# Optimization experiments

Measured on AMD Instinct MI355X. Metric: run time of the kernel, lower is better.

Reference implementation:

```python
import jax, jax.numpy as jnp
import numpy as np
from jax import lax

H = 32          # hidden per direction (HIDDENDIM // 2)
T = 8192        # tokens
M = 12          # morphemes per token
INP = 100       # word2vec dim (LSTMINPDIM)
DP_V, DPD = 40, 4
TAGS = 44


def _lstm_dir(x, h0, c0, Wih, Whh, b, reverse):
    """Single-direction LSTM over x: [S, D]. PyTorch gate order i,f,g,o."""
    def step(carry, xt):
        h, c = carry
        g = xt @ Wih.T + h @ Whh.T + b
        i, f, gg, o = jnp.split(g, 4, axis=-1)
        c = jax.nn.sigmoid(f) * c + jax.nn.sigmoid(i) * jnp.tanh(gg)
        h = jax.nn.sigmoid(o) * jnp.tanh(c)
        return (h, c), h
    xs = jnp.flip(x, 0) if reverse else x
    (hN, cN), hs = lax.scan(step, (h0, c0), xs)
    if reverse:
        hs = jnp.flip(hs, 0)
    return hs, hN, cN


def _bilstm(x, h0, c0, layers):
    """2-layer bidirectional LSTM. h0/c0: [4, H], PyTorch order (layer*2+dir).
    layers: list of (Wih[2,4H,Din], Whh[2,4H,H], b[2,4H]) per layer (b = b_ih+b_hh)."""
    out = x
    hs, cs = [], []
    for l, (Wih, Whh, b) in enumerate(layers):
        f_hs, f_h, f_c = _lstm_dir(out, h0[2 * l], c0[2 * l], Wih[0], Whh[0], b[0], False)
        b_hs, b_h, b_c = _lstm_dir(out, h0[2 * l + 1], c0[2 * l + 1], Wih[1], Whh[1], b[1], True)
        out = jnp.concatenate([f_hs, b_hs], axis=-1)
        hs += [f_h, b_h]
        cs += [f_c, b_c]
    return out, jnp.stack(hs), jnp.stack(cs)


def setup_inputs() -> dict:
    key = jax.random.key(0)
    ks = jax.random.split(key, 20)
    k = 1.0 / np.sqrt(H)
    u = lambda kk, shp: jax.random.uniform(kk, shp, jnp.float32, -k, k)
    inp = {
        "morp_embs": jax.random.normal(ks[0], (T, M, INP), jnp.float32),
        "feat_vectors": jax.random.uniform(ks[1], (T, 1), jnp.float32),
        "dp_emb": jax.random.normal(ks[2], (DP_V, DPD), jnp.float32),
        "m_Wih0": u(ks[3], (2, 4 * H, INP)),
        "m_Whh0": u(ks[4], (2, 4 * H, H)),
        "m_b0": u(ks[5], (2, 4 * H)),
        "m_Wih1": u(ks[6], (2, 4 * H, 2 * H)),
        "m_Whh1": u(ks[7], (2, 4 * H, H)),
        "m_b1": u(ks[8], (2, 4 * H)),
        "t_Wih0": u(ks[9], (2, 4 * H, 2 * H + DPD + 1)),
        "t_Whh0": u(ks[10], (2, 4 * H, H)),
        "t_b0": u(ks[11], (2, 4 * H)),
        "t_Wih1": u(ks[12], (2, 4 * H, 2 * H)),
        "t_Whh1": u(ks[13], (2, 4 * H, H)),
        "t_b1": u(ks[14], (2, 4 * H)),
        "W_out": u(ks[15], (TAGS, 2 * H)),
        "b_out": u(ks[16], (TAGS,)),
        "dp_in": jax.random.randint(ks[17], (T,), 0, DP_V, jnp.int32),
        "mask": jax.random.randint(ks[18], (T,), 0, 2, jnp.int32),
    }
    return inp


def reference(morp_embs, feat_vectors, dp_emb,
              m_Wih0, m_Whh0, m_b0, m_Wih1, m_Whh1, m_b1,
              t_Wih0, t_Whh0, t_b0, t_Wih1, t_Whh1, t_b1,
              W_out, b_out, dp_in, mask):
    dtype = morp_embs.dtype
    morp_layers = [(m_Wih0, m_Whh0, m_b0), (m_Wih1, m_Whh1, m_b1)]
    tok_layers = [(t_Wih0, t_Whh0, t_b0), (t_Wih1, t_Whh1, t_b1)]
    z = jnp.zeros((4, H), dtype)

    # morpheme-level LSTM: hidden state is carried across tokens, as in the
    # original (self.hidden_lstm_morp is threaded through the python loop)
    def tok_step(carry, xm):
        h, c = carry
        out, hN, cN = _bilstm(xm, h, c, morp_layers)   # out: [M, 2H]
        return (hN, cN), out[-1]                        # last morpheme output

    _, tok_vec = lax.scan(tok_step, (z, z), morp_embs)  # [T, 2H]

    input_embs = jnp.concatenate([tok_vec, dp_emb[dp_in], feat_vectors], axis=1)  # [T, 69]
    tok_out, _, _ = _bilstm(input_embs, z, z, tok_layers)  # [T, 2H]

    tag_space = tok_out @ W_out.T + b_out  # [T, TAGS]
    # where mask <= 0, force last logit to 1 (pre-relu), as in the python loop
    tag_space = tag_space.at[:, -1].set(
        jnp.where(mask > 0, tag_space[:, -1], jnp.asarray(1.0, dtype)))
    tag_space = jax.nn.relu(tag_space)
    return jax.nn.softmax(tag_space, axis=1)
```

## Files before the change

### kernel.cpp

```cpp
#include <hip/hip_runtime.h>

#define T_TOK   8192
#define M_MORPH 12
#define NMORPH  (T_TOK * M_MORPH)

typedef float f32x4 __attribute__((ext_vector_type(4)));
typedef float f32x2 __attribute__((ext_vector_type(2)));
typedef short s16x8 __attribute__((ext_vector_type(8)));

__device__ __forceinline__ float sigmoidf_(float x) {
    return __fdividef(1.f, 1.f + __expf(-x));
}

__device__ __forceinline__ int rowof(int s, int mode, int N) {
    if (mode == 0) return s;
    if (mode == 1) { int m = s % M_MORPH; return s + (M_MORPH - 1) - 2 * m; }
    return N - 1 - s;
}

#define PKFMA(acc, w, h) \
    asm("v_pk_fma_f32 %0, %1, %2, %0" : "+v"(acc) : "v"(w), "v"(h))

__device__ __forceinline__ void half_swap(float v, float& lo_b, float& hi_b) {
#if __has_builtin(__builtin_amdgcn_permlane32_swap)
    auto r = __builtin_amdgcn_permlane32_swap(__float_as_uint(v), __float_as_uint(v),
                                              false, false);
    lo_b = __uint_as_float((unsigned)r[0]);
    hi_b = __uint_as_float((unsigned)r[1]);
#else
    const float e = __shfl_xor(v, 32);
    const bool lo = ((threadIdx.x & 63) < 32);
    lo_b = lo ? v : e;
    hi_b = lo ? e : v;
#endif
}

__global__ void prep_B(const float* __restrict__ W, const float* __restrict__ b,
                       unsigned short* __restrict__ Bh, unsigned short* __restrict__ Bl,
                       float* __restrict__ bcat, int WK, int KPAD) {
    const int n = blockIdx.x;
    const int k = threadIdx.x;
    const int dir = n >> 7, r = n & 127;
    float v = (k < WK) ? W[(size_t)(dir * 128 + r) * WK + k] : 0.f;
    unsigned int u = __float_as_uint(v);
    unsigned short hb = (unsigned short)(u >> 16);
    float fh = __uint_as_float(u & 0xFFFF0000u);
    float lo = v - fh;
    unsigned short lb = (unsigned short)(__float_as_uint(lo) >> 16);
    Bh[(size_t)n * KPAD + k] = hb;
    Bl[(size_t)n * KPAD + k] = lb;
    if (k == 0) bcat[n] = b[dir * 128 + r];
}

template <int KACT, int KPAD, int AS>
__global__ __launch_bounds__(256, 2) void gemm_mfma(const float* __restrict__ A,
                                                    const unsigned short* __restrict__ Bh,
                                                    const unsigned short* __restrict__ Bl,
                                                    const float* __restrict__ bc,
                                                    float* __restrict__ X) {
    const int lane = threadIdx.x & 63;
    const int wave = threadIdx.x >> 6;
    const int col = lane & 15;
    const int kc  = (lane >> 4) * 8;
    const int row0 = blockIdx.x * 128 + wave * 32;

    f32x4 acc[2][16];
#pragma unroll
    for (int ct = 0; ct < 16; ++ct) {
        const float bv = bc[ct * 16 + col];
        f32x4 v; v[0] = bv; v[1] = bv; v[2] = bv; v[3] = bv;
        acc[0][ct] = v; acc[1][ct] = v;
    }

    const float* a0 = A + (size_t)(row0 + col) * AS;
    const float* a1 = A + (size_t)(row0 + 16 + col) * AS;

#pragma unroll
    for (int ks = 0; ks < KPAD / 32; ++ks) {
        const int kb = ks * 32 + kc;
        s16x8 ah[2], al[2];
#pragma unroll
        for (int rt = 0; rt < 2; ++rt) {
            const float* ap = (rt ? a1 : a0) + kb;
            float av[8];
#pragma unroll
            for (int h = 0; h < 2; ++h) {
                float4 t; t.x = t.y = t.z = t.w = 0.f;
                if ((ks + 1) * 32 <= KACT || kb + h * 4 < KACT)
                    t = *(const float4*)(ap + h * 4);
                av[h * 4 + 0] = t.x; av[h * 4 + 1] = t.y;
                av[h * 4 + 2] = t.z; av[h * 4 + 3] = t.w;
            }
#pragma unroll
            for (int j = 0; j < 8; ++j) {
                const unsigned int u = __float_as_uint(av[j]);
                const unsigned short hb = (unsigned short)(u >> 16);
                const float fh = __uint_as_float(u & 0xFFFF0000u);
                const float lov = av[j] - fh;
                const unsigned short lb = (unsigned short)(__float_as_uint(lov) >> 16);
                ah[rt][j] = (short)hb;
                al[rt][j] = (short)lb;
            }
        }

        const unsigned short* bhp = Bh + (size_t)col * KPAD + kb;
        const unsigned short* blp = Bl + (size_t)col * KPAD + kb;
#pragma unroll
        for (int ct = 0; ct < 16; ++ct) {
            const s16x8 bh8 = *(const s16x8*)(bhp + (size_t)ct * 16 * KPAD);
            const s16x8 bl8 = *(const s16x8*)(blp + (size_t)ct * 16 * KPAD);
#pragma unroll
            for (int rt = 0; rt < 2; ++rt) {
                acc[rt][ct] = __builtin_amdgcn_mfma_f32_16x16x32_bf16(ah[rt], bh8, acc[rt][ct], 0, 0, 0);
                acc[rt][ct] = __builtin_amdgcn_mfma_f32_16x16x32_bf16(ah[rt], bl8, acc[rt][ct], 0, 0, 0);
                acc[rt][ct] = __builtin_amdgcn_mfma_f32_16x16x32_bf16(al[rt], bh8, acc[rt][ct], 0, 0, 0);
            }
        }
    }

    const int r_in = (lane >> 4) * 4;
#pragma unroll
    for (int rt = 0; rt < 2; ++rt)
#pragma unroll
        for (int g = 0; g < 2; ++g)
#pragma unroll
            for (int ct2 = 0; ct2 < 4; ++ct2) {
                const int ct = g * 8 + ct2;
                const int c  = ct * 16 + col;
                const int cm = c & 127;
                const int nc = g * 128 + cm * 2;
#pragma unroll
                for (int i = 0; i < 4; ++i) {
                    f32x2 v2;
                    v2[0] = acc[rt][ct][i];
                    v2[1] = acc[rt][ct + 4][i];
                    *(f32x2*)&X[(size_t)(row0 + rt * 16 + r_in + i) * 256 + nc] = v2;
                }
            }
}

template <int DM, int SL>
__device__ __forceinline__ void chain_body(
    const float* __restrict__ Xc, float* __restrict__ HoutLane,
    const bool lo, const int lane,
    f32x2 (&wa)[16], f32x2 (&wb)[16], float* sh,
    const int N, const int cs, const int ce, const int ws)
{
    const float cg = lo ? 2.f : 1.f;
    const float ca = lo ? -1.f : 0.f;

    f32x2 q[8];
#pragma unroll
    for (int p = 0; p < 8; ++p) {
        const int rp = rowof(ws + p, DM, N);
        q[p] = *(const f32x2*)(Xc + (size_t)rp * 256);
    }

    int mp = (ws + 8) % M_MORPH;
    int pb;
    {
        const int sp0 = ws + 8;
        int rp0;
        if (DM == 1)      rp0 = sp0 + 11 - 2 * mp;
        else if (DM == 2) rp0 = N - 1 - sp0;
        else              rp0 = sp0;
        pb = rp0 * 1024;
    }

    int ms = ws % M_MORPH;
    int rs;
    if (DM == 1)      rs = ws + 11 - 2 * ms;
    else if (DM == 2) rs = N - 1 - ws;
    else              rs = ws;
    int tk = ws / M_MORPH;

    float hreg = 0.f, c = 0.f;

#pragma unroll 1
    for (int s = ws; s < ce; s += 8) {
#pragma unroll
        for (int u = 0; u < 8; ++u) {
            const int su = s + u;
            const float x1 = q[u][0], x2 = q[u][1];

            {
                const int sp = su + 8;
                const int ob = (sp < ce) ? pb : 0;
                q[u] = *(const f32x2*)((const char*)Xc + ob);
                if (DM == 1) {
                    if (mp == 11) { mp = 0; pb += 23 * 1024; }
                    else          { ++mp; pb -= 1024; }
                } else if (DM == 2) { pb -= 1024; }
                else                { pb += 1024; }
            }

            sh[lane] = hreg;
            f32x4 hq[8];
            {
                const f32x4* s4 = (const f32x4*)sh;
#pragma unroll
                for (int i = 0; i < 8; ++i) hq[i] = s4[i];
            }

            f32x2 a01 = {x1, 0.f}, a23 = {0.f, 0.f};
            f32x2 b01 = {x2, 0.f}, b23 = {0.f, 0.f};
#pragma unroll
            for (int i = 0; i < 8; ++i) {
                f32x2 hlo = __builtin_shufflevector(hq[i], hq[i], 0, 1);
                f32x2 hhi = __builtin_shufflevector(hq[i], hq[i], 2, 3);
                PKFMA(a01, wa[2 * i],     hlo);
                PKFMA(a23, wa[2 * i + 1], hhi);
                PKFMA(b01, wb[2 * i],     hlo);
                PKFMA(b23, wb[2 * i + 1], hhi);
            }
            const float g1 = (a01[0] + a01[1]) + (a23[0] + a23[1]);
            const float g2 = (b01[0] + b01[1]) + (b23[0] + b23[1]);

            const float s1 = sigmoidf_(g1);
            const float uu = sigmoidf_(cg * g2);
            const float t2 = fmaf(cg, uu, ca);

            float si, sf, tg, so;
            half_swap(s1, si, sf);
            half_swap(t2, tg, so);

            c = sf * c + si * tg;
            const float th = 2.f * sigmoidf_(2.f * c) - 1.f;
            hreg = so * th;

            if (!SL) {
                if (su >= cs) {
                    if (lo) HoutLane[(size_t)rs * 64] = hreg;
                }
            } else {
                const bool last = (DM == 1) ? (ms == 0) : (ms == 11);
                if (su >= cs && last) {
                    if (lo) HoutLane[(size_t)tk * 64] = hreg;
                }
            }

            if (DM == 1) {
                if (ms == 11) { ms = 0; ++tk; rs += 23; }
                else          { ++ms; --rs; }
            } else if (DM == 2) {
                --rs;
            } else {
                ++rs;
                if (SL) { if (ms == 11) { ms = 0; ++tk; } else ++ms; }
            }
        }
    }
}

template <int BDM, int SL>
__global__ __launch_bounds__(64)
__attribute__((amdgpu_waves_per_eu(2, 2)))
void lstm_chain_t(const float* __restrict__ Xall,
                  const float* __restrict__ Whhall,
                  float* __restrict__ Hout,
                  int N, int Lc, int Wu) {
    __shared__ __align__(16) float sh[64];
    const int lane = threadIdx.x;
    const int dir = blockIdx.y;
    const float* Whh = Whhall + dir * 128 * 32;

    const int cs = blockIdx.x * Lc;
    if (cs >= N) return;
    int ce = cs + Lc; if (ce > N) ce = N;
    int ws = cs - Wu; if (ws < 0) ws = 0;

    f32x2 wa[16], wb[16];
    {
        const f32x2* w1 = (const f32x2*)(Whh + lane * 32);
        const f32x2* w2 = (const f32x2*)(Whh + (lane + 64) * 32);
#pragma unroll
        for (int i = 0; i < 16; ++i) { wa[i] = w1[i]; wb[i] = w2[i]; }
    }
#pragma unroll
    for (int i = 0; i < 16; ++i) {
        asm volatile("" : "+v"(wa[i]));
        asm volatile("" : "+v"(wb[i]));
    }

    const float* Xc = Xall + dir * 128 + lane * 2;
    float* HoutLane = Hout + dir * 32 + lane;
    const bool lo = (lane < 32);

    if (dir == 0)
        chain_body<0,   SL>(Xc, HoutLane, lo, lane, wa, wb, sh, N, cs, ce, ws);
    else
        chain_body<BDM, SL>(Xc, HoutLane, lo, lane, wa, wb, sh, N, cs, ce, ws);
}

__global__ __launch_bounds__(256) void build_embs(const float* __restrict__ tokvec,
                                                  const float* __restrict__ dp_emb,
                                                  const int* __restrict__ dp_in,
                                                  const float* __restrict__ feat,
                                                  float* __restrict__ embs) {
    const int idx = blockIdx.x * 256 + threadIdx.x;
    if (idx >= T_TOK * 96) return;
    const int t = idx / 96, i = idx % 96;
    float v;
    if (i < 64)      v = tokvec[(size_t)t * 64 + i];
    else if (i < 68) v = dp_emb[dp_in[t] * 4 + (i - 64)];
    else if (i == 68) v = feat[t];
    else             v = 0.f;
    embs[idx] = v;
}

__global__ __launch_bounds__(256) void epilogue_k(const float* __restrict__ Ht1,
                                                  const float* __restrict__ Wout,
                                                  const float* __restrict__ bout,
                                                  const int* __restrict__ maskp,
                                                  float* __restrict__ out) {
    const int wid = threadIdx.x >> 6;
    const int lane = threadIdx.x & 63;
    const int t = blockIdx.x * 4 + wid;
    float acc = -1e30f;
    if (lane < 44) {
        acc = bout[lane];
        const float* wr = Wout + lane * 64;
        const float* hr = Ht1 + (size_t)t * 64;
#pragma unroll
        for (int k = 0; k < 64; ++k) acc += hr[k] * wr[k];
        if (lane == 43 && maskp[t] <= 0) acc = 1.0f;
        acc = fmaxf(acc, 0.f);
    }
    float mx = acc;
#pragma unroll
    for (int off = 32; off >= 1; off >>= 1) mx = fmaxf(mx, __shfl_xor(mx, off));
    const float e = (lane < 44) ? __expf(acc - mx) : 0.f;
    float ssum = e;
#pragma unroll
    for (int off = 32; off >= 1; off >>= 1) ssum += __shfl_xor(ssum, off);
    if (lane < 44) out[(size_t)t * 44 + lane] = e / ssum;
}

extern "C" void kernel_launch(void* const* d_in, const int* in_sizes, int n_in,
                              void* d_out, int out_size, void* d_ws, size_t ws_size,
                              hipStream_t stream) {
    const float* morp  = (const float*)d_in[0];
    const float* feat  = (const float*)d_in[1];
    const float* dpemb = (const float*)d_in[2];
    const float* mWih0 = (const float*)d_in[3];
    const float* mWhh0 = (const float*)d_in[4];
    const float* mb0   = (const float*)d_in[5];
    const float* mWih1 = (const float*)d_in[6];
    const float* mWhh1 = (const float*)d_in[7];
    const float* mb1   = (const float*)d_in[8];
    const float* tWih0 = (const float*)d_in[9];
    const float* tWhh0 = (const float*)d_in[10];
    const float* tb0   = (const float*)d_in[11];
    const float* tWih1 = (const float*)d_in[12];
    const float* tWhh1 = (const float*)d_in[13];
    const float* tb1   = (const float*)d_in[14];
    const float* Wout  = (const float*)d_in[15];
    const float* bout  = (const float*)d_in[16];
    const int*   dpin  = (const int*)d_in[17];
    const int*   maskp = (const int*)d_in[18];
    float* out = (float*)d_out;

    float* w = (float*)d_ws;
    size_t off = 0;
    float* X0     = w + off; off += (size_t)NMORPH * 256;
    float* Hcat0  = w + off; off += (size_t)NMORPH * 64;
    float* tokvec = w + off; off += (size_t)T_TOK * 64;
    float* embs   = w + off; off += (size_t)T_TOK * 96;
    float* Ht0    = w + off; off += (size_t)T_TOK * 64;
    float* Ht1    = w + off; off += (size_t)T_TOK * 64;
    unsigned short* Bh = (unsigned short*)(w + off); off += 256 * 128 / 2;
    unsigned short* Bl = (unsigned short*)(w + off); off += 256 * 128 / 2;
    float* bcat   = w + off; off += 256;
    float* Xt = X0;
    (void)ws_size; (void)in_sizes; (void)n_in; (void)out_size;

    prep_B<<<256, 128, 0, stream>>>(mWih0, mb0, Bh, Bl, bcat, 100, 128);
    gemm_mfma<100, 128, 100><<<NMORPH / 128, 256, 0, stream>>>(morp, Bh, Bl, bcat, X0);
    lstm_chain_t<1, 0><<<dim3(NMORPH / 96, 2), 64, 0, stream>>>(X0, mWhh0, Hcat0, NMORPH, 96, 64);
    prep_B<<<256, 64, 0, stream>>>(mWih1, mb1, Bh, Bl, bcat, 64, 64);
    gemm_mfma<64, 64, 64><<<NMORPH / 128, 256, 0, stream>>>(Hcat0, Bh, Bl, bcat, X0);
    lstm_chain_t<1, 1><<<dim3(NMORPH / 96, 2), 64, 0, stream>>>(X0, mWhh1, tokvec, NMORPH, 96, 64);

    build_embs<<<(T_TOK * 96) / 256, 256, 0, stream>>>(tokvec, dpemb, dpin, feat, embs);
    prep_B<<<256, 96, 0, stream>>>(tWih0, tb0, Bh, Bl, bcat, 69, 96);
    gemm_mfma<96, 96, 96><<<T_TOK / 128, 256, 0, stream>>>(embs, Bh, Bl, bcat, Xt);
    lstm_chain_t<2, 0><<<dim3(T_TOK / 32, 2), 64, 0, stream>>>(Xt, tWhh0, Ht0, T_TOK, 32, 64);
    prep_B<<<256, 64, 0, stream>>>(tWih1, tb1, Bh, Bl, bcat, 64, 64);
    gemm_mfma<64, 64, 64><<<T_TOK / 128, 256, 0, stream>>>(Ht0, Bh, Bl, bcat, Xt);
    lstm_chain_t<2, 0><<<dim3(T_TOK / 32, 2), 64, 0, stream>>>(Xt, tWhh1, Ht1, T_TOK, 32, 64);

    epilogue_k<<<T_TOK / 4, 256, 0, stream>>>(Ht1, Wout, bout, maskp, out);
}
```

Before: 405.9 us.

## Batch morpheme LSTM recurrences into MFMA across 16 chunks per wave

Replaces the per-lane scalar packed-FMA recurrence for the two morpheme-level LSTM layers with a new kernel in which each wave runs 16 independent sequence chunks as the columns of bf16 split-precision MFMAs (hi/lo split of Whh and h). The hidden state is redistributed through a small LDS tile each step, the gate inputs are prefetched two steps ahead, and inactive steps during warmup are written to a dump buffer. The GEMM gains a template flag so the morpheme path stores X in natural column order, matching the new kernel's layout. This aims to cut the serial FMA work and launch far fewer waves. In exchange it adds LDS round-trips and bf16 split conversion on every step, plus three MFMAs per gate tile.

```diff
diff --git a/kernel.cpp b/kernel.cpp
--- a/kernel.cpp
+++ b/kernel.cpp
@@ -33,6 +33,17 @@
     lo_b = lo ? v : e;
     hi_b = lo ? e : v;
 #endif
+}
+
+__device__ __forceinline__ void bf16_split_pair(float x0, float x1,
+                                                unsigned& hi, unsigned& lo) {
+    const unsigned u0 = __float_as_uint(x0);
+    const unsigned u1 = __float_as_uint(x1);
+    hi = (u0 >> 16) | (u1 & 0xFFFF0000u);
+    const float h0 = __uint_as_float(u0 & 0xFFFF0000u);
+    const float h1 = __uint_as_float(u1 & 0xFFFF0000u);
+    lo = (__float_as_uint(x0 - h0) >> 16)
+       | (__float_as_uint(x1 - h1) & 0xFFFF0000u);
 }
 
 __global__ void prep_B(const float* __restrict__ W, const float* __restrict__ b,
@@ -52,7 +63,7 @@
     if (k == 0) bcat[n] = b[dir * 128 + r];
 }
 
-template <int KACT, int KPAD, int AS>
+template <int KACT, int KPAD, int AS, bool PAIRED>
 __global__ __launch_bounds__(256, 2) void gemm_mfma(const float* __restrict__ A,
                                                     const unsigned short* __restrict__ Bh,
                                                     const unsigned short* __restrict__ Bl,
@@ -119,24 +130,212 @@
     }
 
     const int r_in = (lane >> 4) * 4;
-#pragma unroll
-    for (int rt = 0; rt < 2; ++rt)
-#pragma unroll
-        for (int g = 0; g < 2; ++g)
-#pragma unroll
-            for (int ct2 = 0; ct2 < 4; ++ct2) {
-                const int ct = g * 8 + ct2;
-                const int c  = ct * 16 + col;
-                const int cm = c & 127;
-                const int nc = g * 128 + cm * 2;
-#pragma unroll
-                for (int i = 0; i < 4; ++i) {
-                    f32x2 v2;
-                    v2[0] = acc[rt][ct][i];
-                    v2[1] = acc[rt][ct + 4][i];
-                    *(f32x2*)&X[(size_t)(row0 + rt * 16 + r_in + i) * 256 + nc] = v2;
+    if constexpr (!PAIRED) {
+#pragma unroll
+        for (int rt = 0; rt < 2; ++rt)
+#pragma unroll
+            for (int ct = 0; ct < 16; ++ct)
+#pragma unroll
+                for (int i = 0; i < 4; ++i)
+                    X[(size_t)(row0 + rt * 16 + r_in + i) * 256 + ct * 16 + col] = acc[rt][ct][i];
+    } else {
+#pragma unroll
+        for (int rt = 0; rt < 2; ++rt)
+#pragma unroll
+            for (int g = 0; g < 2; ++g)
+#pragma unroll
+                for (int ct2 = 0; ct2 < 4; ++ct2) {
+                    const int ct = g * 8 + ct2;
+                    const int c  = ct * 16 + col;
+                    const int cm = c & 127;
+                    const int nc = g * 128 + cm * 2;
+#pragma unroll
+                    for (int i = 0; i < 4; ++i) {
+                        f32x2 v2;
+                        v2[0] = acc[rt][ct][i];
+                        v2[1] = acc[rt][ct + 4][i];
+                        *(f32x2*)&X[(size_t)(row0 + rt * 16 + r_in + i) * 256 + nc] = v2;
+                    }
                 }
-            }
+    }
+}
+
+template <int DM, int SL>
+__device__ __forceinline__ void mstep(
+    const char* __restrict__ xb, char* __restrict__ hb,
+    float* __restrict__ dl, float* __restrict__ Hls,
+    const int col, const int rg,
+    const s16x8 (&wh)[8], const s16x8 (&wl)[8],
+    s16x8& bh, s16x8& bl,
+    f32x4 (&q)[8], f32x4 (&cst)[2],
+    int& su, const int cs, const int ce,
+    int& pf_b, int& m_pf,
+    int& st_b, int& m_st, int& tk_b)
+{
+    f32x4 acc[8];
+#pragma unroll
+    for (int tt = 0; tt < 8; ++tt) {
+        acc[tt] = __builtin_amdgcn_mfma_f32_16x16x32_bf16(wh[tt], bh, q[tt], 0, 0, 0);
+        acc[tt] = __builtin_amdgcn_mfma_f32_16x16x32_bf16(wh[tt], bl, acc[tt], 0, 0, 0);
+        acc[tt] = __builtin_amdgcn_mfma_f32_16x16x32_bf16(wl[tt], bh, acc[tt], 0, 0, 0);
+    }
+
+    {
+        const char* xp = xb + pf_b;
+#pragma unroll
+        for (int tt = 0; tt < 8; ++tt)
+            q[tt] = *(const f32x4*)(xp + tt * 64);
+        if (DM == 1) {
+            const bool w = (m_pf == 11);
+            pf_b += w ? 23 * 1024 : -1024;
+            m_pf = w ? 0 : m_pf + 1;
+        } else {
+            pf_b += 1024;
+        }
+    }
+
+    f32x4 v0, v1;
+#pragma unroll
+    for (int p = 0; p < 2; ++p) {
+#pragma unroll
+        for (int r = 0; r < 4; ++r) {
+            const float gi = acc[0 + p][r], gf = acc[2 + p][r];
+            const float gg = acc[4 + p][r], go = acc[6 + p][r];
+            const float si = sigmoidf_(gi);
+            const float sf = sigmoidf_(gf);
+            const float tg = 2.f * sigmoidf_(2.f * gg) - 1.f;
+            const float so = sigmoidf_(go);
+            const float cn = sf * cst[p][r] + si * tg;
+            cst[p][r] = cn;
+            const float th = 2.f * sigmoidf_(2.f * cn) - 1.f;
+            const float hv = so * th;
+            if (p == 0) v0[r] = hv; else v1[r] = hv;
+        }
+    }
+
+    {
+        bool act = (su >= cs) && (su < ce);
+        if (SL) act = act && ((DM == 1) ? (m_st == 0) : (m_st == 11));
+        char* base = hb + (SL ? tk_b : st_b);
+        float* a0 = act ? (float*)base : dl;
+        float* a1 = act ? (float*)(base + 64) : (dl + 4);
+        *(f32x4*)a0 = v0;
+        *(f32x4*)a1 = v1;
+
+        ++su;
+        if (DM == 1) {
+            const bool w = (m_st == 11);
+            st_b += w ? 23 * 256 : -256;
+            if (SL) tk_b += w ? 256 : 0;
+            m_st = w ? 0 : m_st + 1;
+        } else {
+            st_b += 256;
+            if (SL) {
+                const bool w = (m_st == 11);
+                tk_b += w ? 256 : 0;
+                m_st = w ? 0 : m_st + 1;
+            }
+        }
+    }
+
+    *(f32x4*)&Hls[col * 36 + 4 * rg]      = v0;
+    *(f32x4*)&Hls[col * 36 + 16 + 4 * rg] = v1;
+    const f32x4 r0 = *(const f32x4*)&Hls[col * 36 + 8 * rg];
+    const f32x4 r1 = *(const f32x4*)&Hls[col * 36 + 8 * rg + 4];
+    union { s16x8 s; unsigned u[4]; } BH, BL;
+    bf16_split_pair(r0[0], r0[1], BH.u[0], BL.u[0]);
+    bf16_split_pair(r0[2], r0[3], BH.u[1], BL.u[1]);
+    bf16_split_pair(r1[0], r1[1], BH.u[2], BL.u[2]);
+    bf16_split_pair(r1[2], r1[3], BH.u[3], BL.u[3]);
+    bh = BH.s; bl = BL.s;
+}
+
+template <int DM, int SL>
+__device__ __forceinline__ void mrun(
+    const float* __restrict__ Xn, const float* __restrict__ Wd,
+    float* __restrict__ Hout, float* __restrict__ dump,
+    float* __restrict__ Hls,
+    const int dir, const int col, const int rg, const int lane,
+    const int N, const int Lc, const int Wu, const int nsteps)
+{
+    const int g  = blockIdx.x * 16 + col;
+    const int cs = g * Lc;
+    const int ce = cs + Lc;
+    const int off = (g == 0) ? 0 : cs - Wu;
+
+    s16x8 wh[8], wl[8];
+#pragma unroll
+    for (int tt = 0; tt < 8; ++tt) {
+        const float* wr = Wd + (size_t)(tt * 16 + col) * 32 + rg * 8;
+        const float4 w0 = *(const float4*)(wr);
+        const float4 w1 = *(const float4*)(wr + 4);
+        union { s16x8 s; unsigned u[4]; } H_, L_;
+        bf16_split_pair(w0.x, w0.y, H_.u[0], L_.u[0]);
+        bf16_split_pair(w0.z, w0.w, H_.u[1], L_.u[1]);
+        bf16_split_pair(w1.x, w1.y, H_.u[2], L_.u[2]);
+        bf16_split_pair(w1.z, w1.w, H_.u[3], L_.u[3]);
+        wh[tt] = H_.s; wl[tt] = L_.s;
+    }
+
+    const char* xb = (const char*)Xn + dir * 512 + rg * 16;
+    char* hb = (char*)Hout + (size_t)(dir * 32 + 4 * rg) * 4;
+    float* dl = dump + ((size_t)(blockIdx.x * 2 + dir) * 64 + lane) * 8;
+
+    int m = off % 12;
+    int rb = ((DM == 1) ? (off + 11 - 2 * m) : off) * 1024;
+    f32x4 q0[8], q1[8];
+    {
+        const char* xp = xb + rb;
+#pragma unroll
+        for (int tt = 0; tt < 8; ++tt) q0[tt] = *(const f32x4*)(xp + tt * 64);
+    }
+    if (DM == 1) { const bool w = (m == 11); rb += w ? 23 * 1024 : -1024; m = w ? 0 : m + 1; }
+    else rb += 1024;
+    {
+        const char* xp = xb + rb;
+#pragma unroll
+        for (int tt = 0; tt < 8; ++tt) q1[tt] = *(const f32x4*)(xp + tt * 64);
+    }
+    int m_pf = m, pf_b = rb;
+    if (DM == 1) { const bool w = (m_pf == 11); pf_b += w ? 23 * 1024 : -1024; m_pf = w ? 0 : m_pf + 1; }
+    else pf_b += 1024;
+
+    int m_st = off % 12;
+    int st_b = ((DM == 1) ? (off + 11 - 2 * m_st) : off) * 256;
+    int tk_b = (off / 12) * 256;
+    int su = off;
+
+    f32x4 cst[2];
+    cst[0][0] = 0.f; cst[0][1] = 0.f; cst[0][2] = 0.f; cst[0][3] = 0.f;
+    cst[1] = cst[0];
+    s16x8 bh = {0, 0, 0, 0, 0, 0, 0, 0};
+    s16x8 bl = {0, 0, 0, 0, 0, 0, 0, 0};
+
+#pragma unroll 1
+    for (int t = 0; t < nsteps; t += 2) {
+        mstep<DM, SL>(xb, hb, dl, Hls, col, rg, wh, wl, bh, bl, q0, cst,
+                      su, cs, ce, pf_b, m_pf, st_b, m_st, tk_b);
+        mstep<DM, SL>(xb, hb, dl, Hls, col, rg, wh, wl, bh, bl, q1, cst,
+                      su, cs, ce, pf_b, m_pf, st_b, m_st, tk_b);
+    }
+}
+
+template <int BDM, int SL>
+__global__ __launch_bounds__(64)
+__attribute__((amdgpu_waves_per_eu(1, 1)))
+void lstm_mfma(const float* __restrict__ Xn, const float* __restrict__ Whhall,
+               float* __restrict__ Hout, float* __restrict__ dump,
+               int N, int Lc, int Wu, int nsteps) {
+    __shared__ __align__(16) float Hls[16 * 36];
+    const int lane = threadIdx.x;
+    const int col = lane & 15, rg = lane >> 4;
+    const int dir = blockIdx.y;
+    const float* Wd = Whhall + (size_t)dir * 128 * 32;
+
+    if (dir == 0)
+        mrun<0,   SL>(Xn, Wd, Hout, dump, Hls, dir, col, rg, lane, N, Lc, Wu, nsteps);
+    else
+        mrun<BDM, SL>(Xn, Wd, Hout, dump, Hls, dir, col, rg, lane, N, Lc, Wu, nsteps);
 }
 
 template <int DM, int SL>
@@ -182,7 +381,6 @@
         for (int u = 0; u < 8; ++u) {
             const int su = s + u;
             const float x1 = q[u][0], x2 = q[u][1];
-
             {
                 const int sp = su + 8;
                 const int ob = (sp < ce) ? pb : 0;
@@ -372,21 +570,22 @@
     unsigned short* Bl = (unsigned short*)(w + off); off += 256 * 128 / 2;
     float* bcat   = w + off; off += 256;
     float* Xt = X0;
+    float* dump = embs;
     (void)ws_size; (void)in_sizes; (void)n_in; (void)out_size;
 
     prep_B<<<256, 128, 0, stream>>>(mWih0, mb0, Bh, Bl, bcat, 100, 128);
-    gemm_mfma<100, 128, 100><<<NMORPH / 128, 256, 0, stream>>>(morp, Bh, Bl, bcat, X0);
-    lstm_chain_t<1, 0><<<dim3(NMORPH / 96, 2), 64, 0, stream>>>(X0, mWhh0, Hcat0, NMORPH, 96, 64);
+    gemm_mfma<100, 128, 100, false><<<NMORPH / 128, 256, 0, stream>>>(morp, Bh, Bl, bcat, X0);
+    lstm_mfma<1, 0><<<dim3(64, 2), 64, 0, stream>>>(X0, mWhh0, Hcat0, dump, NMORPH, 96, 64, 160);
     prep_B<<<256, 64, 0, stream>>>(mWih1, mb1, Bh, Bl, bcat, 64, 64);
-    gemm_mfma<64, 64, 64><<<NMORPH / 128, 256, 0, stream>>>(Hcat0, Bh, Bl, bcat, X0);
-    lstm_chain_t<1, 1><<<dim3(NMORPH / 96, 2), 64, 0, stream>>>(X0, mWhh1, tokvec, NMORPH, 96, 64);
+    gemm_mfma<64, 64, 64, false><<<NMORPH / 128, 256, 0, stream>>>(Hcat0, Bh, Bl, bcat, X0);
+    lstm_mfma<1, 1><<<dim3(64, 2), 64, 0, stream>>>(X0, mWhh1, tokvec, dump, NMORPH, 96, 64, 160);
 
     build_embs<<<(T_TOK * 96) / 256, 256, 0, stream>>>(tokvec, dpemb, dpin, feat, embs);
     prep_B<<<256, 96, 0, stream>>>(tWih0, tb0, Bh, Bl, bcat, 69, 96);
-    gemm_mfma<96, 96, 96><<<T_TOK / 128, 256, 0, stream>>>(embs, Bh, Bl, bcat, Xt);
+    gemm_mfma<96, 96, 96, true><<<T_TOK / 128, 256, 0, stream>>>(embs, Bh, Bl, bcat, Xt);
     lstm_chain_t<2, 0><<<dim3(T_TOK / 32, 2), 64, 0, stream>>>(Xt, tWhh0, Ht0, T_TOK, 32, 64);
     prep_B<<<256, 64, 0, stream>>>(tWih1, tb1, Bh, Bl, bcat, 64, 64);
-    gemm_mfma<64, 64, 64><<<T_TOK / 128, 256, 0, stream>>>(Ht0, Bh, Bl, bcat, Xt);
+    gemm_mfma<64, 64, 64, true><<<T_TOK / 128, 256, 0, stream>>>(Ht0, Bh, Bl, bcat, Xt);
     lstm_chain_t<2, 0><<<dim3(T_TOK / 32, 2), 64, 0, stream>>>(Xt, tWhh1, Ht1, T_TOK, 32, 64);
 
     epilogue_k<<<T_TOK / 4, 256, 0, stream>>>(Ht1, Wout, bout, maskp, out);
```

New measurement: 795.5 us. 1.96x slower.
